# Kernel tuning notes

Hardware: AMD Instinct MI355X
Metric: run time of the kernel (lower is better)

The kernel has to match this reference:

```python
import jax, jax.numpy as jnp
import numpy as np

DIM = 1024
N = 8192


def setup_inputs() -> dict:
    key = jax.random.key(0)
    k_x, k_w, k_b = jax.random.split(key, 3)
    inputs = jax.random.normal(k_x, (N, DIM), dtype=jnp.float32)
    # nn.Bilinear(dimension, dimension, 1): weight shape (1, d, d), bias shape (1,)
    bound = 1.0 / np.sqrt(DIM)
    W = jax.random.uniform(k_w, (DIM, DIM), jnp.float32, -bound, bound)
    b = jax.random.uniform(k_b, (1,), jnp.float32, -bound, bound)
    return {"inputs": inputs, "W": W, "b": b}


def reference(inputs, W, b):
    # out[i, j] = inputs[i] @ W @ inputs[j] + b  ==  (X @ W) @ X^T + b
    # Algebraically identical to repeat+nn.Bilinear, without the N^2*d blowup.
    xw = inputs @ W              # (N, d)
    out = xw @ inputs.T + b[0]   # (N, N)
    return out
```

## Files before the change

### kernel.cpp

```cpp
#include <hip/hip_runtime.h>
#include <hip/hip_bf16.h>

typedef __bf16 bf16;
typedef __bf16 bf16x8 __attribute__((ext_vector_type(8)));
typedef __bf16 bf16x4 __attribute__((ext_vector_type(4)));
typedef float  f32x4  __attribute__((ext_vector_type(4)));

#define GLD_LDS(g, l)                                                        \
  __builtin_amdgcn_global_load_lds(                                          \
      (const __attribute__((address_space(1))) void*)(g),                    \
      (__attribute__((address_space(3))) void*)(l), 16, 0, 0)

template <int EPI>
__global__ void gemm_bt(const bf16* __restrict__ A, const bf16* __restrict__ B,
                        bf16* __restrict__ Cb, float* __restrict__ Cf,
                        const float* __restrict__ bias_p,
                        int M, int N, int K) {
  __shared__ bf16 As[128 * 32];
  __shared__ bf16 Bs[128 * 32];

  const int tid  = threadIdx.x;
  const int lane = tid & 63;
  const int wave = tid >> 6;
  const int wr = wave >> 1;
  const int wc = wave & 1;
  const int fr = lane & 15;
  const int fq = lane >> 4;

  const int row0 = blockIdx.y * 128;
  const int col0 = blockIdx.x * 128;

  f32x4 acc[4][4] = {};

  const int c0 = tid, c1 = 256 + tid;
  const bf16* Ag0 = A + (size_t)(row0 + (c0 >> 2)) * K + (c0 & 3) * 8;
  const bf16* Ag1 = A + (size_t)(row0 + (c1 >> 2)) * K + (c1 & 3) * 8;
  const bf16* Bg0 = B + (size_t)(col0 + (c0 >> 2)) * K + (c0 & 3) * 8;
  const bf16* Bg1 = B + (size_t)(col0 + (c1 >> 2)) * K + (c1 & 3) * 8;
  bf16* Al0 = As + (wave * 64) * 8;
  bf16* Al1 = As + (256 + wave * 64) * 8;
  bf16* Bl0 = Bs + (wave * 64) * 8;
  bf16* Bl1 = Bs + (256 + wave * 64) * 8;

  for (int k0 = 0; k0 < K; k0 += 32) {
    GLD_LDS(Ag0 + k0, Al0);
    GLD_LDS(Ag1 + k0, Al1);
    GLD_LDS(Bg0 + k0, Bl0);
    GLD_LDS(Bg1 + k0, Bl1);
    __syncthreads();

    bf16x8 af[4], bg[4];
#pragma unroll
    for (int m = 0; m < 4; ++m)
      af[m] = *(const bf16x8*)&As[(wr * 64 + m * 16 + fr) * 32 + fq * 8];
#pragma unroll
    for (int n = 0; n < 4; ++n)
      bg[n] = *(const bf16x8*)&Bs[(wc * 64 + n * 16 + fr) * 32 + fq * 8];

#pragma unroll
    for (int m = 0; m < 4; ++m)
#pragma unroll
      for (int n = 0; n < 4; ++n)
        acc[m][n] = __builtin_amdgcn_mfma_f32_16x16x32_bf16(af[m], bg[n],
                                                            acc[m][n], 0, 0, 0);
    __syncthreads();
  }

  const float bias = (EPI == 1) ? bias_p[0] : 0.0f;
#pragma unroll
  for (int m = 0; m < 4; ++m) {
#pragma unroll
    for (int n = 0; n < 4; ++n) {
      const int r  = row0 + wr * 64 + m * 16 + fq * 4;
      const int cc = col0 + wc * 64 + n * 16 + fr;
#pragma unroll
      for (int j = 0; j < 4; ++j) {
        if (EPI == 1)
          Cf[(size_t)(r + j) * N + cc] = acc[m][n][j] + bias;
        else
          Cb[(size_t)(r + j) * N + cc] = (bf16)acc[m][n][j];
      }
    }
  }
}

__global__ void cvt_f32_bf16(const float* __restrict__ in, bf16* __restrict__ out,
                             int n4) {
  int i = blockIdx.x * blockDim.x + threadIdx.x;
  if (i >= n4) return;
  const float4 v = ((const float4*)in)[i];
  bf16x4 o;
  o[0] = (bf16)v.x; o[1] = (bf16)v.y; o[2] = (bf16)v.z; o[3] = (bf16)v.w;
  ((bf16x4*)out)[i] = o;
}

__global__ void transpose_cvt_w(const float* __restrict__ W, bf16* __restrict__ Wt) {
  __shared__ float s[32][33];
  const int tx = threadIdx.x & 31;
  const int ty = threadIdx.x >> 5;
  const int n0 = blockIdx.x * 32;
  const int k0 = blockIdx.y * 32;
#pragma unroll
  for (int p = 0; p < 4; ++p)
    s[ty + p * 8][tx] = W[(size_t)(k0 + ty + p * 8) * 1024 + n0 + tx];
  __syncthreads();
#pragma unroll
  for (int p = 0; p < 4; ++p)
    Wt[(size_t)(n0 + ty + p * 8) * 1024 + k0 + tx] = (bf16)s[tx][ty + p * 8];
}

extern "C" void kernel_launch(void* const* d_in, const int* in_sizes, int n_in,
                              void* d_out, int out_size, void* d_ws, size_t ws_size,
                              hipStream_t stream) {
  const float* X = (const float*)d_in[0];
  const float* W = (const float*)d_in[1];
  const float* b = (const float*)d_in[2];
  float* out = (float*)d_out;

  const int Nn = 8192, D = 1024;

  char* ws = (char*)d_ws;
  bf16* Xb  = (bf16*)(ws);
  bf16* XWb = (bf16*)(ws + (size_t)16 * 1024 * 1024);
  bf16* Wt  = (bf16*)(ws + (size_t)32 * 1024 * 1024);

  cvt_f32_bf16<<<(Nn * D / 4 + 255) / 256, 256, 0, stream>>>(X, Xb, Nn * D / 4);
  transpose_cvt_w<<<dim3(D / 32, D / 32), 256, 0, stream>>>(W, Wt);
  gemm_bt<0><<<dim3(D / 128, Nn / 128), 256, 0, stream>>>(Xb, Wt, XWb, nullptr,
                                                          nullptr, Nn, D, D);
  gemm_bt<1><<<dim3(Nn / 128, Nn / 128), 256, 0, stream>>>(XWb, Xb, nullptr, out,
                                                           b, Nn, Nn, D);
}
```

Measured before the change: 218.1 us.

## Add 256x256 double-buffered swizzled-LDS GEMM for the large N×N product

```diff
diff --git a/kernel.cpp b/kernel.cpp
--- a/kernel.cpp
+++ b/kernel.cpp
@@ -11,27 +11,145 @@
       (const __attribute__((address_space(1))) void*)(g),                    \
       (__attribute__((address_space(3))) void*)(l), 16, 0, 0)
 
-template <int EPI>
+#define BAR()   asm volatile("s_barrier" ::: "memory")
+#define WLG()   asm volatile("s_waitcnt lgkmcnt(0)" ::: "memory")
+#define WVM4()  asm volatile("s_waitcnt vmcnt(4)" ::: "memory")
+#define WVM0()  asm volatile("s_waitcnt vmcnt(0)" ::: "memory")
+#define PRIO1() __builtin_amdgcn_s_setprio(1)
+#define PRIO0() __builtin_amdgcn_s_setprio(0)
+
+__global__ __launch_bounds__(512, 2)
+void gemm256(const bf16* __restrict__ A, const bf16* __restrict__ B,
+             float* __restrict__ C, const float* __restrict__ bias_p,
+             int M, int N, int K) {
+  extern __shared__ bf16 lds[];
+  const int tid  = threadIdx.x;
+  const int lane = tid & 63, wave = tid >> 6;
+  const int wm = wave >> 2, wn = wave & 3;
+  const int fr = lane & 15, fq = lane >> 4;
+  const int xm = (fr & 7) << 4;
+
+  const int nwg = gridDim.x;
+  const int bid = blockIdx.x;
+  const int swz = (bid & 7) * (nwg >> 3) + (bid >> 3);
+  const int gx  = N >> 8;
+  const int row0 = (swz / gx) << 8, col0 = (swz % gx) << 8;
+
+  const int srow = wave * 8 + (lane >> 3);
+  const int scol = ((lane & 7) ^ (lane >> 3)) * 8;
+  const bf16* Agl = A + (size_t)(row0 + srow) * K + scol;
+  const bf16* Bgl = B + (size_t)(col0 + srow) * K + scol;
+
+#define STG(gl, tb, t, h)                                                    \
+  do {                                                                       \
+    const size_t _k = (size_t)(t) * 64;                                      \
+    GLD_LDS((gl) + (size_t)((h) * 128) * K + _k,                             \
+            lds + (tb) + ((t) & 1) * 16384 + (h) * 8192 + wave * 512);       \
+    GLD_LDS((gl) + (size_t)((h) * 128 + 64) * K + _k,                        \
+            lds + (tb) + ((t) & 1) * 16384 + (h) * 8192 + 4096 + wave * 512);\
+  } while (0)
+
+  const char* ldsc = (const char*)lds;
+  const int acol0 = (fq * 16) ^ xm, acol1 = (64 + fq * 16) ^ xm;
+
+  f32x4  acc[8][4] = {};
+  bf16x8 af[4][2], bg[2][2];
+
+#define LDA(mg, p)                                                           \
+  do {                                                                       \
+    _Pragma("unroll") for (int m_ = 0; m_ < 4; ++m_) {                       \
+      const int r_ = (wm * 128 + ((mg) * 4 + m_) * 16 + fr) * 128;           \
+      af[m_][0] = *(const bf16x8*)(ldsc + (p) * 32768 + r_ + acol0);         \
+      af[m_][1] = *(const bf16x8*)(ldsc + (p) * 32768 + r_ + acol1);         \
+    }                                                                        \
+  } while (0)
+
+#define LDB(np, p)                                                           \
+  do {                                                                       \
+    _Pragma("unroll") for (int n_ = 0; n_ < 2; ++n_) {                       \
+      const int r_ = (wn * 64 + ((np) * 2 + n_) * 16 + fr) * 128;            \
+      bg[n_][0] = *(const bf16x8*)(ldsc + 65536 + (p) * 32768 + r_ + acol0); \
+      bg[n_][1] = *(const bf16x8*)(ldsc + 65536 + (p) * 32768 + r_ + acol1); \
+    }                                                                        \
+  } while (0)
+
+#define MM(mg, np)                                                           \
+  do {                                                                       \
+    _Pragma("unroll") for (int kk_ = 0; kk_ < 2; ++kk_)                      \
+      _Pragma("unroll") for (int m_ = 0; m_ < 4; ++m_)                       \
+        _Pragma("unroll") for (int n_ = 0; n_ < 2; ++n_)                     \
+          acc[(mg) * 4 + m_][(np) * 2 + n_] =                                \
+              __builtin_amdgcn_mfma_f32_16x16x32_bf16(                       \
+                  af[m_][kk_], bg[n_][kk_],                                  \
+                  acc[(mg) * 4 + m_][(np) * 2 + n_], 0, 0, 0);               \
+  } while (0)
+
+  STG(Agl, 0, 0, 0); STG(Agl, 0, 0, 1);
+  STG(Bgl, 32768, 0, 0); STG(Bgl, 32768, 0, 1);
+  STG(Agl, 0, 1, 0); STG(Agl, 0, 1, 1);
+  WVM4(); BAR();
+
+  const int NT = K >> 6;
+  for (int T = 0; T < NT; T += 2) {
+    const bool s2 = (T + 2 < NT), s3 = (T + 3 < NT);
+    LDA(0, 0); LDB(0, 0);
+    STG(Bgl, 32768, T + 1, 0);
+    BAR(); WLG(); PRIO1(); MM(0, 0); PRIO0(); BAR();
+    LDB(1, 0);
+    STG(Bgl, 32768, T + 1, 1);
+    BAR(); WLG(); PRIO1(); MM(0, 1); PRIO0(); BAR();
+    LDA(1, 0); LDB(0, 0);
+    BAR(); WLG(); PRIO1(); MM(1, 0); PRIO0(); BAR();
+    LDB(1, 0);
+    if (s2) { STG(Agl, 0, T + 2, 0); STG(Agl, 0, T + 2, 1); }
+    BAR(); WLG(); PRIO1(); MM(1, 1); PRIO0();
+    if (s2) { WVM4(); } else { WVM0(); }
+    BAR();
+    LDA(0, 1); LDB(0, 1);
+    if (s2) STG(Bgl, 32768, T + 2, 0);
+    BAR(); WLG(); PRIO1(); MM(0, 0); PRIO0(); BAR();
+    LDB(1, 1);
+    if (s2) STG(Bgl, 32768, T + 2, 1);
+    BAR(); WLG(); PRIO1(); MM(0, 1); PRIO0(); BAR();
+    LDA(1, 1); LDB(0, 1);
+    BAR(); WLG(); PRIO1(); MM(1, 0); PRIO0(); BAR();
+    LDB(1, 1);
+    if (s3) { STG(Agl, 0, T + 3, 0); STG(Agl, 0, T + 3, 1); }
+    BAR(); WLG(); PRIO1(); MM(1, 1); PRIO0();
+    if (s3) { WVM4(); } else { WVM0(); }
+    BAR();
+  }
+
+  const float bias = bias_p[0];
+#pragma unroll
+  for (int m = 0; m < 8; ++m) {
+#pragma unroll
+    for (int n = 0; n < 4; ++n) {
+      const int r = row0 + wm * 128 + m * 16 + fq * 4;
+      const int c = col0 + wn * 64 + n * 16 + fr;
+#pragma unroll
+      for (int j = 0; j < 4; ++j)
+        C[(size_t)(r + j) * N + c] = acc[m][n][j] + bias;
+    }
+  }
+#undef STG
+#undef LDA
+#undef LDB
+#undef MM
+}
+
 __global__ void gemm_bt(const bf16* __restrict__ A, const bf16* __restrict__ B,
-                        bf16* __restrict__ Cb, float* __restrict__ Cf,
-                        const float* __restrict__ bias_p,
-                        int M, int N, int K) {
+                        bf16* __restrict__ Cb, int M, int N, int K) {
   __shared__ bf16 As[128 * 32];
   __shared__ bf16 Bs[128 * 32];
-
   const int tid  = threadIdx.x;
   const int lane = tid & 63;
   const int wave = tid >> 6;
-  const int wr = wave >> 1;
-  const int wc = wave & 1;
-  const int fr = lane & 15;
-  const int fq = lane >> 4;
-
-  const int row0 = blockIdx.y * 128;
-  const int col0 = blockIdx.x * 128;
+  const int wr = wave >> 1, wc = wave & 1;
+  const int fr = lane & 15, fq = lane >> 4;
+  const int row0 = blockIdx.y * 128, col0 = blockIdx.x * 128;
 
   f32x4 acc[4][4] = {};
-
   const int c0 = tid, c1 = 256 + tid;
   const bf16* Ag0 = A + (size_t)(row0 + (c0 >> 2)) * K + (c0 & 3) * 8;
   const bf16* Ag1 = A + (size_t)(row0 + (c1 >> 2)) * K + (c1 & 3) * 8;
@@ -48,40 +166,31 @@
     GLD_LDS(Bg0 + k0, Bl0);
     GLD_LDS(Bg1 + k0, Bl1);
     __syncthreads();
-
-    bf16x8 af[4], bg[4];
+    bf16x8 af[4], bgf[4];
 #pragma unroll
     for (int m = 0; m < 4; ++m)
       af[m] = *(const bf16x8*)&As[(wr * 64 + m * 16 + fr) * 32 + fq * 8];
 #pragma unroll
     for (int n = 0; n < 4; ++n)
-      bg[n] = *(const bf16x8*)&Bs[(wc * 64 + n * 16 + fr) * 32 + fq * 8];
-
+      bgf[n] = *(const bf16x8*)&Bs[(wc * 64 + n * 16 + fr) * 32 + fq * 8];
 #pragma unroll
     for (int m = 0; m < 4; ++m)
 #pragma unroll
       for (int n = 0; n < 4; ++n)
-        acc[m][n] = __builtin_amdgcn_mfma_f32_16x16x32_bf16(af[m], bg[n],
+        acc[m][n] = __builtin_amdgcn_mfma_f32_16x16x32_bf16(af[m], bgf[n],
                                                             acc[m][n], 0, 0, 0);
     __syncthreads();
   }
-
-  const float bias = (EPI == 1) ? bias_p[0] : 0.0f;
-#pragma unroll
-  for (int m = 0; m < 4; ++m) {
+#pragma unroll
+  for (int m = 0; m < 4; ++m)
 #pragma unroll
     for (int n = 0; n < 4; ++n) {
       const int r  = row0 + wr * 64 + m * 16 + fq * 4;
       const int cc = col0 + wc * 64 + n * 16 + fr;
 #pragma unroll
-      for (int j = 0; j < 4; ++j) {
-        if (EPI == 1)
-          Cf[(size_t)(r + j) * N + cc] = acc[m][n][j] + bias;
-        else
-          Cb[(size_t)(r + j) * N + cc] = (bf16)acc[m][n][j];
-      }
+      for (int j = 0; j < 4; ++j)
+        Cb[(size_t)(r + j) * N + cc] = (bf16)acc[m][n][j];
     }
-  }
 }
 
 __global__ void cvt_f32_bf16(const float* __restrict__ in, bf16* __restrict__ out,
@@ -118,7 +227,6 @@
   float* out = (float*)d_out;
 
   const int Nn = 8192, D = 1024;
-
   char* ws = (char*)d_ws;
   bf16* Xb  = (bf16*)(ws);
   bf16* XWb = (bf16*)(ws + (size_t)16 * 1024 * 1024);
@@ -126,8 +234,7 @@
 
   cvt_f32_bf16<<<(Nn * D / 4 + 255) / 256, 256, 0, stream>>>(X, Xb, Nn * D / 4);
   transpose_cvt_w<<<dim3(D / 32, D / 32), 256, 0, stream>>>(W, Wt);
-  gemm_bt<0><<<dim3(D / 128, Nn / 128), 256, 0, stream>>>(Xb, Wt, XWb, nullptr,
-                                                          nullptr, Nn, D, D);
-  gemm_bt<1><<<dim3(Nn / 128, Nn / 128), 256, 0, stream>>>(XWb, Xb, nullptr, out,
-                                                           b, Nn, Nn, D);
-}
+  gemm_bt<<<dim3(D / 128, Nn / 128), 256, 0, stream>>>(Xb, Wt, XWb, Nn, D, D);
+  gemm256<<<(Nn / 256) * (Nn / 256), 512, 131072, stream>>>(XWb, Xb, out, b,
+                                                            Nn, Nn, D);
+}
```

New measurement: 208.8 us. 1.04x faster.

## Rewrite GEMM as 256x256 tile, 8-wave, double-buffered ping-pong pipeline

Applied to the files above, without the earlier changes.

```diff
diff --git a/kernel.cpp b/kernel.cpp
--- a/kernel.cpp
+++ b/kernel.cpp
@@ -11,77 +11,132 @@
       (const __attribute__((address_space(1))) void*)(g),                    \
       (__attribute__((address_space(3))) void*)(l), 16, 0, 0)
 
+#define SB()    __builtin_amdgcn_s_barrier()
+#define LG0()   asm volatile("s_waitcnt lgkmcnt(0)" ::: "memory")
+#define WVM(n)  asm volatile("s_waitcnt vmcnt(" #n ")" ::: "memory")
+#define PRIO1() __builtin_amdgcn_s_setprio(1)
+#define PRIO0() __builtin_amdgcn_s_setprio(0)
+
 template <int EPI>
-__global__ void gemm_bt(const bf16* __restrict__ A, const bf16* __restrict__ B,
-                        bf16* __restrict__ Cb, float* __restrict__ Cf,
-                        const float* __restrict__ bias_p,
-                        int M, int N, int K) {
-  __shared__ bf16 As[128 * 32];
-  __shared__ bf16 Bs[128 * 32];
+__global__ __launch_bounds__(512, 2)
+void gemm8p(const bf16* __restrict__ A, const bf16* __restrict__ B,
+            bf16* __restrict__ Cb, float* __restrict__ Cf,
+            const float* __restrict__ bias_p, int M, int N, int K) {
+  extern __shared__ bf16 lds[];
+  const int tid  = threadIdx.x;
+  const int lane = tid & 63, wave = tid >> 6;
+  const int wm = wave >> 2, wn = wave & 3;
+  const int fr = lane & 15, fq = lane >> 4;
+  const int gl = (fr + (fr >> 2)) & 3;
+  const int slotb = ((fq ^ gl) << 4);
 
-  const int tid  = threadIdx.x;
-  const int lane = tid & 63;
-  const int wave = tid >> 6;
-  const int wr = wave >> 1;
-  const int wc = wave & 1;
-  const int fr = lane & 15;
-  const int fq = lane >> 4;
+  const int nwg = gridDim.x;
+  const int bid = blockIdx.x;
+  const int swz = (bid & 7) * (nwg >> 3) + (bid >> 3);
+  const int gx  = N >> 8;
+  const int row0 = (swz / gx) << 8, col0 = (swz % gx) << 8;
 
-  const int row0 = blockIdx.y * 128;
-  const int col0 = blockIdx.x * 128;
+  const int gsrc  = ((tid >> 2) + (tid >> 4)) & 3;
+  const int chunk = (tid & 3) ^ gsrc;
+  const int srow  = tid >> 2;
+  const bf16* Agl = A + (size_t)(row0 + srow) * K + chunk * 8;
+  const bf16* Bgl = B + (size_t)(col0 + srow) * K + chunk * 8;
 
-  f32x4 acc[4][4] = {};
+#define STGH(gl_, tb, t, kk)                                                 \
+  do {                                                                       \
+    const size_t _k = (size_t)(t) * 64 + (kk) * 32;                          \
+    GLD_LDS((gl_) + _k,                                                      \
+            lds + (tb) + ((t) & 1) * 16384 + (kk) * 8192 + wave * 512);      \
+    GLD_LDS((gl_) + (size_t)128 * K + _k,                                    \
+            lds + (tb) + ((t) & 1) * 16384 + (kk) * 8192 + 4096 + wave * 512);\
+  } while (0)
 
-  const int c0 = tid, c1 = 256 + tid;
-  const bf16* Ag0 = A + (size_t)(row0 + (c0 >> 2)) * K + (c0 & 3) * 8;
-  const bf16* Ag1 = A + (size_t)(row0 + (c1 >> 2)) * K + (c1 & 3) * 8;
-  const bf16* Bg0 = B + (size_t)(col0 + (c0 >> 2)) * K + (c0 & 3) * 8;
-  const bf16* Bg1 = B + (size_t)(col0 + (c1 >> 2)) * K + (c1 & 3) * 8;
-  bf16* Al0 = As + (wave * 64) * 8;
-  bf16* Al1 = As + (256 + wave * 64) * 8;
-  bf16* Bl0 = Bs + (wave * 64) * 8;
-  bf16* Bl1 = Bs + (256 + wave * 64) * 8;
+  const char* ldsc = (const char*)lds;
+  const char* Ab = ldsc + wm * 8192 + fr * 64 + slotb;
+  const char* Bb = ldsc + 65536 + wn * 4096 + fr * 64 + slotb;
 
-  for (int k0 = 0; k0 < K; k0 += 32) {
-    GLD_LDS(Ag0 + k0, Al0);
-    GLD_LDS(Ag1 + k0, Al1);
-    GLD_LDS(Bg0 + k0, Bl0);
-    GLD_LDS(Bg1 + k0, Bl1);
-    __syncthreads();
+  f32x4  acc[8][4] = {};
+  bf16x8 af[4], bg[4];
 
-    bf16x8 af[4], bg[4];
-#pragma unroll
-    for (int m = 0; m < 4; ++m)
-      af[m] = *(const bf16x8*)&As[(wr * 64 + m * 16 + fr) * 32 + fq * 8];
-#pragma unroll
-    for (int n = 0; n < 4; ++n)
-      bg[n] = *(const bf16x8*)&Bs[(wc * 64 + n * 16 + fr) * 32 + fq * 8];
+#define LDAQ(mg, kk, p)                                                      \
+  do {                                                                       \
+    _Pragma("unroll") for (int m_ = 0; m_ < 4; ++m_)                         \
+      af[m_] = *(const bf16x8*)(Ab + (p) * 32768 + (kk) * 16384 +            \
+                                (mg) * 4096 + m_ * 1024);                    \
+  } while (0)
 
-#pragma unroll
-    for (int m = 0; m < 4; ++m)
-#pragma unroll
-      for (int n = 0; n < 4; ++n)
-        acc[m][n] = __builtin_amdgcn_mfma_f32_16x16x32_bf16(af[m], bg[n],
-                                                            acc[m][n], 0, 0, 0);
-    __syncthreads();
+#define LDBQ(kk, p)                                                          \
+  do {                                                                       \
+    _Pragma("unroll") for (int n_ = 0; n_ < 4; ++n_)                         \
+      bg[n_] = *(const bf16x8*)(Bb + (p) * 32768 + (kk) * 16384 + n_ * 1024);\
+  } while (0)
+
+#define MMQ(mg)                                                              \
+  do {                                                                       \
+    _Pragma("unroll") for (int m_ = 0; m_ < 4; ++m_)                         \
+      _Pragma("unroll") for (int n_ = 0; n_ < 4; ++n_)                       \
+        acc[(mg) * 4 + m_][n_] = __builtin_amdgcn_mfma_f32_16x16x32_bf16(    \
+            af[m_], bg[n_], acc[(mg) * 4 + m_][n_], 0, 0, 0);                \
+  } while (0)
+
+  STGH(Agl, 0, 0, 0); STGH(Bgl, 32768, 0, 0);
+  STGH(Agl, 0, 0, 1); STGH(Bgl, 32768, 0, 1);
+  WVM(0); SB();
+
+  const int NT = K >> 6;
+  for (int T = 0; T < NT; T += 2) {
+    const bool s2 = (T + 2 < NT);
+    LDAQ(0, 0, 0); LDBQ(0, 0);
+    STGH(Agl, 0, T + 1, 0);
+    SB(); LG0(); PRIO1(); MMQ(0); PRIO0(); SB();
+    LDAQ(1, 0, 0);
+    STGH(Bgl, 32768, T + 1, 0);
+    SB(); LG0(); PRIO1(); MMQ(1); PRIO0(); WVM(4); SB();
+    LDAQ(0, 1, 0); LDBQ(1, 0);
+    STGH(Agl, 0, T + 1, 1);
+    SB(); LG0(); PRIO1(); MMQ(0); PRIO0(); SB();
+    LDAQ(1, 1, 0);
+    STGH(Bgl, 32768, T + 1, 1);
+    SB(); LG0(); PRIO1(); MMQ(1); PRIO0(); WVM(4); SB();
+    LDAQ(0, 0, 1); LDBQ(0, 1);
+    if (s2) STGH(Agl, 0, T + 2, 0);
+    SB(); LG0(); PRIO1(); MMQ(0); PRIO0(); SB();
+    LDAQ(1, 0, 1);
+    if (s2) STGH(Bgl, 32768, T + 2, 0);
+    SB(); LG0(); PRIO1(); MMQ(1); PRIO0();
+    if (s2) { WVM(4); } else { WVM(0); }
+    SB();
+    LDAQ(0, 1, 1); LDBQ(1, 1);
+    if (s2) STGH(Agl, 0, T + 2, 1);
+    SB(); LG0(); PRIO1(); MMQ(0); PRIO0(); SB();
+    LDAQ(1, 1, 1);
+    if (s2) STGH(Bgl, 32768, T + 2, 1);
+    SB(); LG0(); PRIO1(); MMQ(1); PRIO0();
+    if (s2) { WVM(4); } else { WVM(0); }
+    SB();
   }
 
   const float bias = (EPI == 1) ? bias_p[0] : 0.0f;
 #pragma unroll
-  for (int m = 0; m < 4; ++m) {
+  for (int m = 0; m < 8; ++m) {
 #pragma unroll
     for (int n = 0; n < 4; ++n) {
-      const int r  = row0 + wr * 64 + m * 16 + fq * 4;
-      const int cc = col0 + wc * 64 + n * 16 + fr;
+      const int r = row0 + wm * 128 + m * 16 + fq * 4;
+      const int c = col0 + wn * 64 + n * 16 + fr;
 #pragma unroll
       for (int j = 0; j < 4; ++j) {
         if (EPI == 1)
-          Cf[(size_t)(r + j) * N + cc] = acc[m][n][j] + bias;
+          __builtin_nontemporal_store(acc[m][n][j] + bias,
+                                      &Cf[(size_t)(r + j) * N + c]);
         else
-          Cb[(size_t)(r + j) * N + cc] = (bf16)acc[m][n][j];
+          Cb[(size_t)(r + j) * N + c] = (bf16)acc[m][n][j];
       }
     }
   }
+#undef STGH
+#undef LDAQ
+#undef LDBQ
+#undef MMQ
 }
 
 __global__ void cvt_f32_bf16(const float* __restrict__ in, bf16* __restrict__ out,
@@ -118,7 +173,6 @@
   float* out = (float*)d_out;
 
   const int Nn = 8192, D = 1024;
-
   char* ws = (char*)d_ws;
   bf16* Xb  = (bf16*)(ws);
   bf16* XWb = (bf16*)(ws + (size_t)16 * 1024 * 1024);
@@ -126,8 +180,8 @@
 
   cvt_f32_bf16<<<(Nn * D / 4 + 255) / 256, 256, 0, stream>>>(X, Xb, Nn * D / 4);
   transpose_cvt_w<<<dim3(D / 32, D / 32), 256, 0, stream>>>(W, Wt);
-  gemm_bt<0><<<dim3(D / 128, Nn / 128), 256, 0, stream>>>(Xb, Wt, XWb, nullptr,
-                                                          nullptr, Nn, D, D);
-  gemm_bt<1><<<dim3(Nn / 128, Nn / 128), 256, 0, stream>>>(XWb, Xb, nullptr, out,
-                                                           b, Nn, Nn, D);
+  gemm8p<0><<<(Nn / 256) * (D / 256), 512, 131072, stream>>>(
+      Xb, Wt, XWb, nullptr, nullptr, Nn, D, D);
+  gemm8p<1><<<(Nn / 256) * (Nn / 256), 512, 131072, stream>>>(
+      XWb, Xb, nullptr, out, b, Nn, Nn, D);
 }
```

Result: no change. 221.0 us (+1.3%).

## Rewrite GEMM with double-buffered LDS pipeline, swizzle, and XCD-aware tile mapping

Applied to the files above, without the earlier changes.

```diff
diff --git a/kernel.cpp b/kernel.cpp
--- a/kernel.cpp
+++ b/kernel.cpp
@@ -11,77 +11,122 @@
       (const __attribute__((address_space(1))) void*)(g),                    \
       (__attribute__((address_space(3))) void*)(l), 16, 0, 0)
 
-template <int EPI>
-__global__ void gemm_bt(const bf16* __restrict__ A, const bf16* __restrict__ B,
-                        bf16* __restrict__ Cb, float* __restrict__ Cf,
-                        const float* __restrict__ bias_p,
-                        int M, int N, int K) {
-  __shared__ bf16 As[128 * 32];
-  __shared__ bf16 Bs[128 * 32];
+#define SB()    __builtin_amdgcn_s_barrier()
+#define WVM(n)  asm volatile("s_waitcnt vmcnt(" #n ")" ::: "memory")
+#define PRIO1() __builtin_amdgcn_s_setprio(1)
+#define PRIO0() __builtin_amdgcn_s_setprio(0)
 
+template <int EPI, int NP>
+__global__ __launch_bounds__(512, 4)
+void gemm128k(const bf16* __restrict__ A, const bf16* __restrict__ B,
+              bf16* __restrict__ Cb, float* __restrict__ Cf,
+              const float* __restrict__ bias_p, int M) {
+  constexpr int KP = 1024;
+  constexpr int NT = KP / 64;
+  extern __shared__ char lds[];
   const int tid  = threadIdx.x;
-  const int lane = tid & 63;
-  const int wave = tid >> 6;
-  const int wr = wave >> 1;
-  const int wc = wave & 1;
-  const int fr = lane & 15;
-  const int fq = lane >> 4;
+  const int lane = tid & 63, wave = tid >> 6;
+  const int wm = wave >> 1, wn = wave & 1;
+  const int fr = lane & 15, fq = lane >> 4;
+  const int slotb = ((fq ^ (fr & 3)) << 4);
 
-  const int row0 = blockIdx.y * 128;
-  const int col0 = blockIdx.x * 128;
+  const int nwg = gridDim.x;
+  const int bid = blockIdx.x;
+  constexpr int gx = NP >> 7;
+  const int nTiles = (M >> 7) * gx;
+  int tr, tc;
+  if (NP == 8192 && nwg == 4096) {
+    const int set = bid >> 9, idx = bid & 511;
+    const int xcd = idx & 7, pos = idx >> 3;
+    tr = (set >> 1) * 16 + (xcd >> 2) * 8 + (pos >> 3);
+    tc = (set & 1) * 32 + (xcd & 3) * 8 + (pos & 7);
+  } else {
+    const int swz = (bid & 7) * (nTiles >> 3) + (bid >> 3);
+    tr = swz / gx; tc = swz % gx;
+  }
+  const int row0 = tr << 7, col0 = tc << 7;
 
-  f32x4 acc[4][4] = {};
+  const int srow  = tid >> 2;
+  const int chunk = (tid & 3) ^ ((tid >> 2) & 3);
+  const bf16* Agl = A + (size_t)(row0 + srow) * KP + chunk * 8;
+  const bf16* Bgl = B + (size_t)(col0 + srow) * KP + chunk * 8;
 
-  const int c0 = tid, c1 = 256 + tid;
-  const bf16* Ag0 = A + (size_t)(row0 + (c0 >> 2)) * K + (c0 & 3) * 8;
-  const bf16* Ag1 = A + (size_t)(row0 + (c1 >> 2)) * K + (c1 & 3) * 8;
-  const bf16* Bg0 = B + (size_t)(col0 + (c0 >> 2)) * K + (c0 & 3) * 8;
-  const bf16* Bg1 = B + (size_t)(col0 + (c1 >> 2)) * K + (c1 & 3) * 8;
-  bf16* Al0 = As + (wave * 64) * 8;
-  bf16* Al1 = As + (256 + wave * 64) * 8;
-  bf16* Bl0 = Bs + (wave * 64) * 8;
-  bf16* Bl1 = Bs + (256 + wave * 64) * 8;
+#define STG1(gp, base_off, t, kk)                                            \
+  GLD_LDS((gp) + (size_t)(t) * 64 + (kk) * 32,                               \
+          lds + (base_off) + ((t) & 1) * 16384 + (kk) * 8192 + wave * 1024)
 
-  for (int k0 = 0; k0 < K; k0 += 32) {
-    GLD_LDS(Ag0 + k0, Al0);
-    GLD_LDS(Ag1 + k0, Al1);
-    GLD_LDS(Bg0 + k0, Bl0);
-    GLD_LDS(Bg1 + k0, Bl1);
-    __syncthreads();
+  const char* Ab = lds + wm * 2048 + fr * 64 + slotb;
+  const char* Bb = lds + 32768 + wn * 4096 + fr * 64 + slotb;
 
-    bf16x8 af[4], bg[4];
-#pragma unroll
-    for (int m = 0; m < 4; ++m)
-      af[m] = *(const bf16x8*)&As[(wr * 64 + m * 16 + fr) * 32 + fq * 8];
-#pragma unroll
-    for (int n = 0; n < 4; ++n)
-      bg[n] = *(const bf16x8*)&Bs[(wc * 64 + n * 16 + fr) * 32 + fq * 8];
+  f32x4  acc[2][4] = {};
+  bf16x8 af[2], bg[4];
 
-#pragma unroll
-    for (int m = 0; m < 4; ++m)
-#pragma unroll
-      for (int n = 0; n < 4; ++n)
-        acc[m][n] = __builtin_amdgcn_mfma_f32_16x16x32_bf16(af[m], bg[n],
-                                                            acc[m][n], 0, 0, 0);
-    __syncthreads();
+#define LDA(kk, p)                                                           \
+  do {                                                                       \
+    _Pragma("unroll") for (int m_ = 0; m_ < 2; ++m_)                         \
+      af[m_] = *(const bf16x8*)(Ab + (p) * 16384 + (kk) * 8192 + m_ * 1024); \
+  } while (0)
+
+#define LDBH(np, kk, p)                                                      \
+  do {                                                                       \
+    _Pragma("unroll") for (int n_ = 0; n_ < 2; ++n_)                         \
+      bg[(np) * 2 + n_] = *(const bf16x8*)(Bb + (p) * 16384 + (kk) * 8192 +  \
+                                           ((np) * 2 + n_) * 1024);          \
+  } while (0)
+
+#define MM(np)                                                               \
+  do {                                                                       \
+    _Pragma("unroll") for (int m_ = 0; m_ < 2; ++m_)                         \
+      _Pragma("unroll") for (int n_ = 0; n_ < 2; ++n_)                       \
+        acc[m_][(np) * 2 + n_] = __builtin_amdgcn_mfma_f32_16x16x32_bf16(    \
+            af[m_], bg[(np) * 2 + n_], acc[m_][(np) * 2 + n_], 0, 0, 0);     \
+  } while (0)
+
+  STG1(Agl, 0, 0, 0); STG1(Bgl, 32768, 0, 0);
+  STG1(Agl, 0, 0, 1); STG1(Bgl, 32768, 0, 1);
+  WVM(2); SB();
+
+  for (int T = 0; T < NT; ++T) {
+    const int p = T & 1;
+    const bool st = (T + 1 < NT);
+    LDA(0, p); LDBH(0, 0, p);
+    if (st) STG1(Agl, 0, T + 1, 0);
+    PRIO1(); MM(0); PRIO0();
+    LDBH(1, 0, p);
+    if (st) STG1(Bgl, 32768, T + 1, 0);
+    PRIO1(); MM(1); PRIO0();
+    if (st) { WVM(2); } else { WVM(0); }
+    SB();
+    LDA(1, p); LDBH(0, 1, p);
+    if (st) STG1(Agl, 0, T + 1, 1);
+    PRIO1(); MM(0); PRIO0();
+    LDBH(1, 1, p);
+    if (st) STG1(Bgl, 32768, T + 1, 1);
+    PRIO1(); MM(1); PRIO0();
+    if (st) { WVM(2); } else { WVM(0); }
+    SB();
   }
 
   const float bias = (EPI == 1) ? bias_p[0] : 0.0f;
 #pragma unroll
-  for (int m = 0; m < 4; ++m) {
+  for (int m = 0; m < 2; ++m) {
 #pragma unroll
     for (int n = 0; n < 4; ++n) {
-      const int r  = row0 + wr * 64 + m * 16 + fq * 4;
-      const int cc = col0 + wc * 64 + n * 16 + fr;
+      const int r = row0 + wm * 32 + m * 16 + fq * 4;
+      const int c = col0 + wn * 64 + n * 16 + fr;
 #pragma unroll
       for (int j = 0; j < 4; ++j) {
         if (EPI == 1)
-          Cf[(size_t)(r + j) * N + cc] = acc[m][n][j] + bias;
+          Cf[(size_t)(r + j) * NP + c] = acc[m][n][j] + bias;
         else
-          Cb[(size_t)(r + j) * N + cc] = (bf16)acc[m][n][j];
+          Cb[(size_t)(r + j) * NP + c] = (bf16)acc[m][n][j];
       }
     }
   }
+#undef STG1
+#undef LDA
+#undef LDBH
+#undef MM
 }
 
 __global__ void cvt_f32_bf16(const float* __restrict__ in, bf16* __restrict__ out,
@@ -118,7 +163,6 @@
   float* out = (float*)d_out;
 
   const int Nn = 8192, D = 1024;
-
   char* ws = (char*)d_ws;
   bf16* Xb  = (bf16*)(ws);
   bf16* XWb = (bf16*)(ws + (size_t)16 * 1024 * 1024);
@@ -126,8 +170,7 @@
 
   cvt_f32_bf16<<<(Nn * D / 4 + 255) / 256, 256, 0, stream>>>(X, Xb, Nn * D / 4);
   transpose_cvt_w<<<dim3(D / 32, D / 32), 256, 0, stream>>>(W, Wt);
-  gemm_bt<0><<<dim3(D / 128, Nn / 128), 256, 0, stream>>>(Xb, Wt, XWb, nullptr,
-                                                          nullptr, Nn, D, D);
-  gemm_bt<1><<<dim3(Nn / 128, Nn / 128), 256, 0, stream>>>(XWb, Xb, nullptr, out,
-                                                           b, Nn, Nn, D);
+  gemm128k<0, 1024><<<512, 512, 65536, stream>>>(Xb, Wt, XWb, nullptr, nullptr,
+                                                 Nn);
+  gemm128k<1, 8192><<<4096, 512, 65536, stream>>>(XWb, Xb, nullptr, out, b, Nn);
 }
```

Result: no change. 214.9 us (-1.5%).
